# Optimization experiments

Hardware: AMD Instinct MI355X
Metric: run time of the kernel (lower is better)

Reference implementation:

```python
import jax, jax.numpy as jnp
import numpy as np

DIM = 1024
H = 16
HD = DIM // H          # 64
WIN = 16
KS = 2 * WIN + 1       # 33
GLOBAL_STRIDE = 64


def rope_cache(T, d):
    half = d // 2
    inv_freq = 1.0 / (10000.0 ** (jnp.arange(half, dtype=jnp.float32) / half))
    angles = jnp.arange(T, dtype=jnp.float32)[:, None] * inv_freq[None, :]  # (T, half)
    return jnp.cos(angles), jnp.sin(angles)


def apply_rope(x, cos, sin):
    # x: (B,H,T,D), interleaved pair rotation, matches torch stack+reshape
    x1 = x[..., 0::2]
    x2 = x[..., 1::2]
    x1c = x1 * cos - x2 * sin
    x2c = x1 * sin + x2 * cos
    return jnp.stack([x1c, x2c], axis=-1).reshape(x.shape)


def setup_inputs() -> dict:
    key = jax.random.key(0)
    ks = jax.random.split(key, 5)
    B, T = 1, 2048
    x = jax.random.normal(ks[0], (B, T, DIM), dtype=jnp.float32)
    Wq = jax.random.normal(ks[1], (DIM, DIM), dtype=jnp.float32) * 0.02
    Wk = jax.random.normal(ks[2], (DIM, DIM), dtype=jnp.float32) * 0.02
    Wv = jax.random.normal(ks[3], (DIM, DIM), dtype=jnp.float32) * 0.02
    Wo = jax.random.normal(ks[4], (DIM, DIM), dtype=jnp.float32) * 0.02
    # every GLOBAL_STRIDE-th token is global (equal count per batch)
    gm = jnp.tile((jnp.arange(T) % GLOBAL_STRIDE == 0)[None, :], (B, 1))
    return {"x": x, "Wq": Wq, "Wk": Wk, "Wv": Wv, "Wo": Wo, "global_mask": gm}


def reference(x, Wq, Wk, Wv, Wo, global_mask):
    B, T, D = x.shape
    scale = 1.0 / np.sqrt(HD).astype(np.float32)

    def proj(W):
        return (x @ W.T).reshape(B, T, H, HD).transpose(0, 2, 1, 3)  # (B,H,T,HD)

    q, k, v = proj(Wq), proj(Wk), proj(Wv)
    cos, sin = rope_cache(T, HD)
    q = apply_rope(q, cos, sin)
    k = apply_rope(k, cos, sin)

    pad = lambda a: jnp.pad(a, ((0, 0), (0, 0), (WIN, WIN), (0, 0)))
    widx = jnp.arange(T)[:, None] + jnp.arange(KS)[None, :]  # (T,KS) into padded axis
    Kw = pad(k)[:, :, widx, :]  # (B,H,T,KS,HD)
    Vw = pad(v)[:, :, widx, :]
    scores_local = jnp.einsum('bhtd,bhtwd->bhtw', q, Kw) * scale

    # global tokens: equal G per batch (see setup), so torch's zero-pad + mask is a no-op
    gm = np.asarray(global_mask)
    gidx = np.nonzero(gm[0])[0]  # same positions every batch row
    Kg = k[:, :, gidx, :]  # (B,H,G,HD)
    Vg = v[:, :, gidx, :]
    scores_global = jnp.einsum('bhtd,bhgd->bhtg', q, Kg) * scale

    attn = jax.nn.softmax(jnp.concatenate([scores_local, scores_global], axis=-1), axis=-1)
    w_local = attn[..., :KS]
    w_global = attn[..., KS:]

    ctx = (jnp.einsum('bhtw,bhtwd->bhtd', w_local, Vw)
           + jnp.einsum('bhtg,bhgd->bhtd', w_global, Vg))
    out = ctx.transpose(0, 2, 1, 3).reshape(B, T, D) @ Wo.T

    # full_attn visualization, replicating torch's slot->column mapping exactly:
    # full_attn[..., t, left:right] = w_local[..., t, :win_len]
    t = jnp.arange(T)
    left = jnp.maximum(t - WIN, 0)[:, None]            # (T,1)
    right = jnp.minimum(t + WIN + 1, T)[:, None]       # (T,1)
    cols = left + jnp.arange(KS)[None, :]              # (T,KS)
    valid = cols < right
    cols_d = jnp.where(valid, cols, T)                 # out-of-range -> dropped
    full = jnp.zeros((B, H, T, T), dtype=x.dtype)
    full = full.at[:, :, t[:, None], cols_d].add(
        jnp.where(valid[None, None], w_local, 0.0), mode='drop')
    full = full.at[:, :, :, gidx].add(w_global)
    return out, full
```

## Files before the change

### kernel.cpp

```cpp
#include <hip/hip_runtime.h>
#include <math.h>

#define TT 2048
#define DIMV 1024
#define NH 16
#define HD 64
#define WIN 16
#define KS 33
#define NG 32
#define NS 65
#define TTILE 32
#define KVROWS 96
#define KVP 65

typedef unsigned short ushort;
typedef __attribute__((ext_vector_type(8))) short short8;
typedef __attribute__((ext_vector_type(8))) unsigned short ushort8;
typedef __attribute__((ext_vector_type(4))) float floatx4;

__device__ inline ushort f2bf(float f) {
  unsigned int u = __float_as_uint(f);
  unsigned int r = (u + 0x7FFFu + ((u >> 16) & 1u)) >> 16;
  return (ushort)r;
}
__device__ inline float bf2f(ushort u) {
  return __uint_as_float(((unsigned int)u) << 16);
}

__device__ __forceinline__ void gload16(const ushort* g, ushort* l) {
  __builtin_amdgcn_global_load_lds(
      (const __attribute__((address_space(1))) void*)g,
      (__attribute__((address_space(3))) void*)l, 16, 0, 0);
}

__global__ __launch_bounds__(256) void cast_kernel(
    const float* __restrict__ x, const float* __restrict__ Wq,
    const float* __restrict__ Wk, const float* __restrict__ Wv,
    const float* __restrict__ Wo,
    ushort* __restrict__ xb, ushort* __restrict__ Wqb, ushort* __restrict__ Wkb,
    ushort* __restrict__ Wvb, ushort* __restrict__ Wob) {
  int i = (blockIdx.x * 256 + threadIdx.x) * 4;
  const int NX = TT * DIMV;
  const int NW = DIMV * DIMV;
  float4 v;
  ushort* dst;
  if (i < NX) {
    v = *(const float4*)(x + i);
    dst = xb + i;
  } else {
    int j = i - NX;
    int w = j >> 20;
    int r = j & (NW - 1);
    const float* src = (w == 0) ? Wq : (w == 1) ? Wk : (w == 2) ? Wv : Wo;
    ushort* db       = (w == 0) ? Wqb : (w == 1) ? Wkb : (w == 2) ? Wvb : Wob;
    v = *(const float4*)(src + r);
    dst = db + r;
  }
  ushort4 o;
  o.x = f2bf(v.x); o.y = f2bf(v.y); o.z = f2bf(v.z); o.w = f2bf(v.w);
  *(ushort4*)dst = o;
}

__global__ __launch_bounds__(256) void gemm_bf16_nt(
    const ushort* __restrict__ A,
    const ushort* __restrict__ B0, const ushort* __restrict__ B1, const ushort* __restrict__ B2,
    void* __restrict__ C0, void* __restrict__ C1, void* __restrict__ C2,
    int rope_n, int c_bf16) {
  const ushort* B = (blockIdx.z == 0) ? B0 : (blockIdx.z == 1) ? B1 : B2;
  void* C         = (blockIdx.z == 0) ? C0 : (blockIdx.z == 1) ? C1 : C2;

  __shared__ __align__(16) ushort As[64 * 128];
  __shared__ __align__(16) ushort Bs[128 * 128];

  const int tid  = threadIdx.x;
  const int lane = tid & 63;
  const int wv   = tid >> 6;
  const int m0   = blockIdx.y * 64;
  const int n0   = blockIdx.x * 128;
  const int l15  = lane & 15;
  const int l7   = lane & 7;
  const int cjb  = lane >> 4;

  const int urow = tid >> 4;
  const int ugc  = (tid & 15) ^ (urow & 7);

  floatx4 acc[4][2];
#pragma unroll
  for (int i = 0; i < 4; i++)
#pragma unroll
    for (int j = 0; j < 2; j++) acc[i][j] = (floatx4){0.f, 0.f, 0.f, 0.f};

  const ushort* Ap = A + (size_t)(m0 + urow) * DIMV + ugc * 8;
  const ushort* Bp = B + (size_t)(n0 + urow) * DIMV + ugc * 8;

  for (int k0 = 0; k0 < DIMV; k0 += 128) {
#pragma unroll
    for (int it = 0; it < 4; it++)
      gload16(Ap + (size_t)(it * 16) * DIMV + k0, &As[(tid + it * 256) * 8]);
#pragma unroll
    for (int it = 0; it < 8; it++)
      gload16(Bp + (size_t)(it * 16) * DIMV + k0, &Bs[(tid + it * 256) * 8]);
    __syncthreads();
#pragma unroll
    for (int kk = 0; kk < 128; kk += 32) {
      const int p = (((kk >> 3) + cjb) ^ l7) << 3;
      short8 af[4], bfr[2];
#pragma unroll
      for (int i = 0; i < 4; i++)
        af[i] = *(const short8*)(&As[(i * 16 + l15) * 128 + p]);
#pragma unroll
      for (int j = 0; j < 2; j++)
        bfr[j] = *(const short8*)(&Bs[(wv * 32 + j * 16 + l15) * 128 + p]);
#pragma unroll
      for (int i = 0; i < 4; i++)
#pragma unroll
        for (int j = 0; j < 2; j++)
          acc[i][j] = __builtin_amdgcn_mfma_f32_16x16x32_bf16(af[i], bfr[j], acc[i][j], 0, 0, 0);
    }
    __syncthreads();
  }

  const int row_in = (lane >> 4) * 4;
  const bool do_rope = ((int)blockIdx.z < rope_n);
  const bool odd = (l15 & 1);
#pragma unroll
  for (int i = 0; i < 4; i++) {
#pragma unroll
    for (int j = 0; j < 2; j++) {
      int m = m0 + i * 16 + row_in;
      int n = n0 + wv * 32 + j * 16 + l15;
      int fi = (n & 63) >> 1;
      float invf_rev =
          __expf(-(float)fi * 0.28782313662425573f) * 0.15915494309189535f;
#pragma unroll
      for (int r = 0; r < 4; r++) {
        float o = acc[i][j][r];
        if (do_rope) {
          float part = __shfl_xor(o, 1);
          float rev = (float)(m + r) * invf_rev;
          float fr = rev - floorf(rev);
          float s, c;
          __sincosf(fr * 6.283185307179586f, &s, &c);
          o = odd ? (part * s + o * c) : (o * c - part * s);
        }
        if (c_bf16)
          ((ushort*)C)[(size_t)(m + r) * DIMV + n] = f2bf(o);
        else
          ((float*)C)[(size_t)(m + r) * DIMV + n] = o;
      }
    }
  }
}

__global__ __launch_bounds__(256) void attn_kernel(
    const ushort* __restrict__ Q, const ushort* __restrict__ Km, const ushort* __restrict__ V,
    ushort* __restrict__ ctxb, float* __restrict__ full) {
  const int t0 = blockIdx.x * TTILE;
  const int h  = blockIdx.y;
  __shared__ float k_s[KVROWS * KVP];
  __shared__ float v_s[KVROWS * KVP];
  __shared__ float q_s[TTILE * HD];
  __shared__ float w_s[TTILE * 66];
  const int tid  = threadIdx.x;
  const int lane = tid & 63;
  const int wv   = tid >> 6;

#pragma unroll
  for (int it = 0; it < 3; it++) {
    int idx = tid + it * 256;
    int row = idx >> 3, c8 = idx & 7;
    int g = (row < 64) ? (t0 - WIN + row) : ((row - 64) * 64);
    bool valid = (row >= 64) || ((unsigned)g < TT);
    ushort8 kv = (ushort8){0, 0, 0, 0, 0, 0, 0, 0}, vv = kv;
    if (valid) {
      kv = *(const ushort8*)(Km + (size_t)g * DIMV + h * HD + c8 * 8);
      vv = *(const ushort8*)(V  + (size_t)g * DIMV + h * HD + c8 * 8);
    }
    int base = row * KVP + c8 * 8;
#pragma unroll
    for (int e = 0; e < 8; e++) {
      k_s[base + e] = bf2f(kv[e]);
      v_s[base + e] = bf2f(vv[e]);
    }
  }
  {
    int row = tid >> 3, c8 = tid & 7;
    ushort8 qv = *(const ushort8*)(Q + (size_t)(t0 + row) * DIMV + h * HD + c8 * 8);
    int base = row * HD + c8 * 8;
#pragma unroll
    for (int e = 0; e < 8; e++) q_s[base + e] = bf2f(qv[e]);
  }
  __syncthreads();

#pragma unroll 2
  for (int i = 0; i < 8; i++) {
    int tl = wv * 8 + i;
    int row = (lane < KS) ? (tl + lane) : (64 + lane - KS);
    const float* qr = q_s + tl * HD;
    const float* kr = k_s + row * KVP;
    float p = 0.f;
#pragma unroll 8
    for (int d = 0; d < HD; d++) p += qr[d] * kr[d];
    p *= 0.125f;
    float p2 = qr[lane] * k_s[95 * KVP + lane];
#pragma unroll
    for (int off = 32; off; off >>= 1) p2 += __shfl_xor(p2, off);
    p2 *= 0.125f;
    float m = p;
#pragma unroll
    for (int off = 32; off; off >>= 1) m = fmaxf(m, __shfl_xor(m, off));
    m = fmaxf(m, p2);
    float e = __expf(p - m);
    float sm = e;
#pragma unroll
    for (int off = 32; off; off >>= 1) sm += __shfl_xor(sm, off);
    float e64 = __expf(p2 - m);
    float inv = 1.0f / (sm + e64);
    w_s[tl * 66 + lane] = e * inv;
    if (lane == 0) w_s[tl * 66 + 64] = e64 * inv;
  }

#pragma unroll 2
  for (int i = 0; i < 8; i++) {
    int tl = wv * 8 + i;
    const float* wrow = w_s + tl * 66;
    float acc = 0.f;
#pragma unroll 8
    for (int s = 0; s < KS; s++) acc += wrow[s] * v_s[(tl + s) * KVP + lane];
#pragma unroll 8
    for (int s = KS; s < NS; s++) acc += wrow[s] * v_s[(31 + s) * KVP + lane];
    ctxb[(size_t)(t0 + tl) * DIMV + h * HD + lane] = f2bf(acc);
  }
  __syncthreads();

  for (int tl = 0; tl < TTILE; tl++) {
    int t = t0 + tl;
    int left = (t - WIN > 0) ? (t - WIN) : 0;
    int right = (t + WIN + 1 < TT) ? (t + WIN + 1) : TT;
    int hi = (left + KS < right) ? (left + KS) : right;
    float* row = full + ((size_t)h * TT + t) * TT;
    const float* wrow = w_s + tl * 66;
#pragma unroll
    for (int rep = 0; rep < 2; rep++) {
      int cb = (tid + rep * 256) * 4;
      floatx4 v4 = (floatx4){0.f, 0.f, 0.f, 0.f};
      if ((cb & 63) == 0) v4.x = wrow[KS + (cb >> 6)];
      if (cb + 3 >= left && cb < hi) {
#pragma unroll
        for (int q = 0; q < 4; q++) {
          int c = cb + q;
          if (c >= left && c < hi) v4[q] += wrow[c - left];
        }
      }
      __builtin_nontemporal_store(v4, (floatx4*)(row + cb));
    }
  }
}

extern "C" void kernel_launch(void* const* d_in, const int* in_sizes, int n_in,
                              void* d_out, int out_size, void* d_ws, size_t ws_size,
                              hipStream_t stream) {
  const float* x  = (const float*)d_in[0];
  const float* Wq = (const float*)d_in[1];
  const float* Wk = (const float*)d_in[2];
  const float* Wv = (const float*)d_in[3];
  const float* Wo = (const float*)d_in[4];

  char* ws = (char*)d_ws;
  ushort* xb   = (ushort*)(ws + 0);
  ushort* Wqb  = (ushort*)(ws + (4ull << 20));
  ushort* Wkb  = (ushort*)(ws + (6ull << 20));
  ushort* Wvb  = (ushort*)(ws + (8ull << 20));
  ushort* Wob  = (ushort*)(ws + (10ull << 20));
  ushort* Qb   = (ushort*)(ws + (12ull << 20));
  ushort* Kb   = (ushort*)(ws + (16ull << 20));
  ushort* Vb   = (ushort*)(ws + (20ull << 20));
  ushort* ctxb = (ushort*)(ws + (24ull << 20));

  float* out  = (float*)d_out;
  float* full = out + (size_t)TT * DIMV;

  cast_kernel<<<6144, 256, 0, stream>>>(x, Wq, Wk, Wv, Wo, xb, Wqb, Wkb, Wvb, Wob);

  gemm_bf16_nt<<<dim3(8, 32, 3), 256, 0, stream>>>(xb, Wqb, Wkb, Wvb, Qb, Kb, Vb, 2, 1);

  attn_kernel<<<dim3(TT / TTILE, NH), 256, 0, stream>>>(Qb, Kb, Vb, ctxb, full);

  gemm_bf16_nt<<<dim3(8, 32, 1), 256, 0, stream>>>(ctxb, Wob, Wob, Wob, out, out, out, 0, 0);
}
```

Before: 374.5 us.

## Move full-attention matrix writes into output GEMM launch to overlap with compute

The attention kernel now saves the softmax weights to a small workspace buffer and no longer writes the dense full attention matrix. A new combined kernel runs the output projection GEMM blocks (z=2) alongside blocks (z<2) that expand the saved weights into the 256 MB full matrix with nontemporal stores. The aim is to overlap the bandwidth-bound matrix write with the compute-bound GEMM and to shorten the attention kernel's tail. The cost is an extra workspace round trip for the weights and a single launch with uneven block types.

New measurement: 376.7 us. Within noise of the previous version (+0.6%).

```diff
diff --git a/kernel.cpp b/kernel.cpp
--- a/kernel.cpp
+++ b/kernel.cpp
@@ -61,13 +61,12 @@
   *(ushort4*)dst = o;
 }
 
-__global__ __launch_bounds__(256) void gemm_bf16_nt(
+__global__ __launch_bounds__(256) void gemm_qkv(
     const ushort* __restrict__ A,
     const ushort* __restrict__ B0, const ushort* __restrict__ B1, const ushort* __restrict__ B2,
-    void* __restrict__ C0, void* __restrict__ C1, void* __restrict__ C2,
-    int rope_n, int c_bf16) {
+    ushort* __restrict__ C0, ushort* __restrict__ C1, ushort* __restrict__ C2) {
   const ushort* B = (blockIdx.z == 0) ? B0 : (blockIdx.z == 1) ? B1 : B2;
-  void* C         = (blockIdx.z == 0) ? C0 : (blockIdx.z == 1) ? C1 : C2;
+  ushort* C       = (blockIdx.z == 0) ? C0 : (blockIdx.z == 1) ? C1 : C2;
 
   __shared__ __align__(16) ushort As[64 * 128];
   __shared__ __align__(16) ushort Bs[128 * 128];
@@ -121,7 +120,7 @@
   }
 
   const int row_in = (lane >> 4) * 4;
-  const bool do_rope = ((int)blockIdx.z < rope_n);
+  const bool do_rope = (blockIdx.z < 2);
   const bool odd = (l15 & 1);
 #pragma unroll
   for (int i = 0; i < 4; i++) {
@@ -143,10 +142,7 @@
           __sincosf(fr * 6.283185307179586f, &s, &c);
           o = odd ? (part * s + o * c) : (o * c - part * s);
         }
-        if (c_bf16)
-          ((ushort*)C)[(size_t)(m + r) * DIMV + n] = f2bf(o);
-        else
-          ((float*)C)[(size_t)(m + r) * DIMV + n] = o;
+        C[(size_t)(m + r) * DIMV + n] = f2bf(o);
       }
     }
   }
@@ -154,7 +150,7 @@
 
 __global__ __launch_bounds__(256) void attn_kernel(
     const ushort* __restrict__ Q, const ushort* __restrict__ Km, const ushort* __restrict__ V,
-    ushort* __restrict__ ctxb, float* __restrict__ full) {
+    ushort* __restrict__ ctxb, float* __restrict__ wbuf) {
   const int t0 = blockIdx.x * TTILE;
   const int h  = blockIdx.y;
   __shared__ float k_s[KVROWS * KVP];
@@ -216,8 +212,15 @@
     for (int off = 32; off; off >>= 1) sm += __shfl_xor(sm, off);
     float e64 = __expf(p2 - m);
     float inv = 1.0f / (sm + e64);
-    w_s[tl * 66 + lane] = e * inv;
-    if (lane == 0) w_s[tl * 66 + 64] = e64 * inv;
+    float wvv = e * inv;
+    size_t wb = ((size_t)h * TT + t0 + tl) * 66;
+    w_s[tl * 66 + lane] = wvv;
+    wbuf[wb + lane] = wvv;
+    if (lane == 0) {
+      float w64 = e64 * inv;
+      w_s[tl * 66 + 64] = w64;
+      wbuf[wb + 64] = w64;
+    }
   }
 
 #pragma unroll 2
@@ -231,18 +234,32 @@
     for (int s = KS; s < NS; s++) acc += wrow[s] * v_s[(31 + s) * KVP + lane];
     ctxb[(size_t)(t0 + tl) * DIMV + h * HD + lane] = f2bf(acc);
   }
-  __syncthreads();
-
-  for (int tl = 0; tl < TTILE; tl++) {
-    int t = t0 + tl;
-    int left = (t - WIN > 0) ? (t - WIN) : 0;
-    int right = (t + WIN + 1 < TT) ? (t + WIN + 1) : TT;
-    int hi = (left + KS < right) ? (left + KS) : right;
-    float* row = full + ((size_t)h * TT + t) * TT;
-    const float* wrow = w_s + tl * 66;
-#pragma unroll
-    for (int rep = 0; rep < 2; rep++) {
-      int cb = (tid + rep * 256) * 4;
+}
+
+__global__ __launch_bounds__(256) void out_fused_kernel(
+    const ushort* __restrict__ A, const ushort* __restrict__ Bw,
+    float* __restrict__ Cout, const float* __restrict__ wbuf,
+    float* __restrict__ full) {
+  __shared__ __align__(16) char smem[49152];
+  const int tid = threadIdx.x;
+
+  if (blockIdx.z < 2) {
+    float* wloc = (float*)smem;
+    const int wb = blockIdx.z * 256 + blockIdx.y * 8 + blockIdx.x;
+    const int r0 = wb * 64;
+    for (int idx = tid; idx < 64 * 66; idx += 256)
+      wloc[idx] = wbuf[(size_t)r0 * 66 + idx];
+    __syncthreads();
+#pragma unroll 4
+    for (int iter = 0; iter < 128; iter++) {
+      int rl = iter >> 1;
+      int rowid = r0 + rl;
+      int t = rowid & (TT - 1);
+      int cb = ((iter & 1) * 256 + tid) * 4;
+      int left = (t - WIN > 0) ? (t - WIN) : 0;
+      int right = (t + WIN + 1 < TT) ? (t + WIN + 1) : TT;
+      int hi = (left + KS < right) ? (left + KS) : right;
+      const float* wrow = wloc + rl * 66;
       floatx4 v4 = (floatx4){0.f, 0.f, 0.f, 0.f};
       if ((cb & 63) == 0) v4.x = wrow[KS + (cb >> 6)];
       if (cb + 3 >= left && cb < hi) {
@@ -252,7 +269,69 @@
           if (c >= left && c < hi) v4[q] += wrow[c - left];
         }
       }
-      __builtin_nontemporal_store(v4, (floatx4*)(row + cb));
+      __builtin_nontemporal_store(v4, (floatx4*)(full + (size_t)rowid * TT + cb));
+    }
+    return;
+  }
+
+  ushort* As = (ushort*)smem;
+  ushort* Bs = (ushort*)(smem + 16384);
+
+  const int lane = tid & 63;
+  const int wv   = tid >> 6;
+  const int m0   = blockIdx.y * 64;
+  const int n0   = blockIdx.x * 128;
+  const int l15  = lane & 15;
+  const int l7   = lane & 7;
+  const int cjb  = lane >> 4;
+  const int urow = tid >> 4;
+  const int ugc  = (tid & 15) ^ (urow & 7);
+
+  floatx4 acc[4][2];
+#pragma unroll
+  for (int i = 0; i < 4; i++)
+#pragma unroll
+    for (int j = 0; j < 2; j++) acc[i][j] = (floatx4){0.f, 0.f, 0.f, 0.f};
+
+  const ushort* Ap = A  + (size_t)(m0 + urow) * DIMV + ugc * 8;
+  const ushort* Bp = Bw + (size_t)(n0 + urow) * DIMV + ugc * 8;
+
+  for (int k0 = 0; k0 < DIMV; k0 += 128) {
+#pragma unroll
+    for (int it = 0; it < 4; it++)
+      gload16(Ap + (size_t)(it * 16) * DIMV + k0, &As[(tid + it * 256) * 8]);
+#pragma unroll
+    for (int it = 0; it < 8; it++)
+      gload16(Bp + (size_t)(it * 16) * DIMV + k0, &Bs[(tid + it * 256) * 8]);
+    __syncthreads();
+#pragma unroll
+    for (int kk = 0; kk < 128; kk += 32) {
+      const int p = (((kk >> 3) + cjb) ^ l7) << 3;
+      short8 af[4], bfr[2];
+#pragma unroll
+      for (int i = 0; i < 4; i++)
+        af[i] = *(const short8*)(&As[(i * 16 + l15) * 128 + p]);
+#pragma unroll
+      for (int j = 0; j < 2; j++)
+        bfr[j] = *(const short8*)(&Bs[(wv * 32 + j * 16 + l15) * 128 + p]);
+#pragma unroll
+      for (int i = 0; i < 4; i++)
+#pragma unroll
+        for (int j = 0; j < 2; j++)
+          acc[i][j] = __builtin_amdgcn_mfma_f32_16x16x32_bf16(af[i], bfr[j], acc[i][j], 0, 0, 0);
+    }
+    __syncthreads();
+  }
+
+  const int row_in = (lane >> 4) * 4;
+#pragma unroll
+  for (int i = 0; i < 4; i++) {
+#pragma unroll
+    for (int j = 0; j < 2; j++) {
+      int m = m0 + i * 16 + row_in;
+      int n = n0 + wv * 32 + j * 16 + l15;
+#pragma unroll
+      for (int r = 0; r < 4; r++) Cout[(size_t)(m + r) * DIMV + n] = acc[i][j][r];
     }
   }
 }
@@ -276,15 +355,16 @@
   ushort* Kb   = (ushort*)(ws + (16ull << 20));
   ushort* Vb   = (ushort*)(ws + (20ull << 20));
   ushort* ctxb = (ushort*)(ws + (24ull << 20));
+  float*  wbuf = (float*)(ws + (28ull << 20));
 
   float* out  = (float*)d_out;
   float* full = out + (size_t)TT * DIMV;
 
   cast_kernel<<<6144, 256, 0, stream>>>(x, Wq, Wk, Wv, Wo, xb, Wqb, Wkb, Wvb, Wob);
 
-  gemm_bf16_nt<<<dim3(8, 32, 3), 256, 0, stream>>>(xb, Wqb, Wkb, Wvb, Qb, Kb, Vb, 2, 1);
-
-  attn_kernel<<<dim3(TT / TTILE, NH), 256, 0, stream>>>(Qb, Kb, Vb, ctxb, full);
-
-  gemm_bf16_nt<<<dim3(8, 32, 1), 256, 0, stream>>>(ctxb, Wob, Wob, Wob, out, out, out, 0, 0);
-}
+  gemm_qkv<<<dim3(8, 32, 3), 256, 0, stream>>>(xb, Wqb, Wkb, Wvb, Qb, Kb, Vb);
+
+  attn_kernel<<<dim3(TT / TTILE, NH), 256, 0, stream>>>(Qb, Kb, Vb, ctxb, wbuf);
+
+  out_fused_kernel<<<dim3(8, 32, 3), 256, 0, stream>>>(ctxb, Wob, out, wbuf, full);
+}
```
